# Kernel optimization log

Measured on AMD Instinct MI355X. Metric: run time of the kernel, lower is better.

## Reference

```python
import jax, jax.numpy as jnp
import numpy as np

STEPS = 200
H = 0.5
N_POP = 100000.0
CLAMP = 100000.0
BATCH = 65536


def setup_inputs() -> dict:
    key = jax.random.key(0)
    k1, k2 = jax.random.split(key)
    # init state [B, 1, 4] = (S, E, I, R); positive values
    init = jax.random.uniform(k1, (BATCH, 1, 4), dtype=jnp.float32) * 1000.0
    # weights mirrors nn.Parameter([100000, 3, 6, 0, 0.5, 0.2, 0.25]) with small noise
    base = jnp.array([100000.0, 3.0, 6.0, 0.0, 0.5, 0.2, 0.25], dtype=jnp.float32)
    weights = base + 0.01 * jax.random.normal(k2, (7,), dtype=jnp.float32)
    return {"init": init, "weights": weights}


def reference(init, weights):
    A, B, C = weights[4], weights[5], weights[6]

    def step(x, _):
        # x: [B, 1, 4]
        s, e, i = x[:, 0, 0], x[:, 0, 1], x[:, 0, 2]
        infl = B * s * (e + i) / N_POP
        d = jnp.stack((-infl, infl - A * e, A * e - C * i, C * i), axis=-1)  # [B, 4]
        x_new = x + H * jnp.clip(d[:, None, :], -CLAMP, CLAMP)  # [B, 1, 4]
        return x_new, x_new

    _, outs = jax.lax.scan(step, init, None, length=STEPS)  # [steps, B, 1, 4]
    return jnp.moveaxis(outs, 0, 1)  # [B, steps, 1, 4]
```

## Files before the change

### kernel.cpp

```cpp
#include <hip/hip_runtime.h>

#define BATCH   65536
#define STEPS   200
#define TCHUNK  8
#define NCHUNK  (STEPS / TCHUNK)
#define BLK     64
#define LSTRIDE 33

__global__ __launch_bounds__(BLK) void seir_kernel(
    const float* __restrict__ init,
    const float* __restrict__ w,
    float* __restrict__ out)
{
    __shared__ float lds[BLK * LSTRIDE];

    const int lane   = threadIdx.x;
    const int base_b = blockIdx.x * BLK;
    const int b      = base_b + lane;

    const float A = w[4];
    const float B = w[5];
    const float C = w[6];
    const float invN = 1.0f / 100000.0f;

    float4 x = reinterpret_cast<const float4*>(init)[b];
    float4* outf4 = reinterpret_cast<float4*>(out);

    for (int chunk = 0; chunk < NCHUNK; ++chunk) {
        #pragma unroll
        for (int tt = 0; tt < TCHUNK; ++tt) {
            float infl = B * x.x * (x.y + x.z) * invN;
            float ae = A * x.y;
            float ci = C * x.z;
            float d0 = -infl;
            float d1 = infl - ae;
            float d2 = ae - ci;
            float d3 = ci;
            d0 = fminf(fmaxf(d0, -100000.0f), 100000.0f);
            d1 = fminf(fmaxf(d1, -100000.0f), 100000.0f);
            d2 = fminf(fmaxf(d2, -100000.0f), 100000.0f);
            d3 = fminf(fmaxf(d3, -100000.0f), 100000.0f);
            x.x += 0.5f * d0;
            x.y += 0.5f * d1;
            x.z += 0.5f * d2;
            x.w += 0.5f * d3;
            const int a = lane * LSTRIDE + tt * 4;
            lds[a + 0] = x.x;
            lds[a + 1] = x.y;
            lds[a + 2] = x.z;
            lds[a + 3] = x.w;
        }
        __syncthreads();

        const int t0 = chunk * TCHUNK;
        #pragma unroll
        for (int k = 0; k < 8; ++k) {
            const int s  = k * BLK + lane;
            const int bb = s >> 3;
            const int j  = s & 7;
            const int a  = bb * LSTRIDE + j * 4;
            float4 v = make_float4(lds[a + 0], lds[a + 1], lds[a + 2], lds[a + 3]);
            outf4[(size_t)(base_b + bb) * STEPS + t0 + j] = v;
        }
        __syncthreads();
    }
}

extern "C" void kernel_launch(void* const* d_in, const int* in_sizes, int n_in,
                              void* d_out, int out_size, void* d_ws, size_t ws_size,
                              hipStream_t stream) {
    const float* init = (const float*)d_in[0];
    const float* w    = (const float*)d_in[1];
    float* out        = (float*)d_out;

    seir_kernel<<<dim3(BATCH / BLK), dim3(BLK), 0, stream>>>(init, w, out);
}
```

Baseline: 204.7 us.

## Split recurrence into checkpoint pass and parallel segment-replay pass

A first kernel runs the full recurrence per batch element and stores the state every 8 steps to workspace. A second kernel launches one block per (segment, batch tile), replays 8 steps from its checkpoint, and writes the output through LDS transposition. This exposes far more parallelism for the 210 MB output write than 1024 64-thread blocks looping serially. It costs an extra ~25 MB checkpoint round trip and a second launch, and falls back to the old single kernel if the workspace is too small. The multiply by 1/N is also folded into B.

New measurement: 213.6 us. 1.04x slower.

```diff
diff --git a/kernel.cpp b/kernel.cpp
--- a/kernel.cpp
+++ b/kernel.cpp
@@ -2,65 +2,117 @@
 
 #define BATCH   65536
 #define STEPS   200
-#define TCHUNK  8
-#define NCHUNK  (STEPS / TCHUNK)
-#define BLK     64
+#define SEG     8
+#define NSEG    (STEPS / SEG)
+#define NCKPT   (NSEG - 1)
 #define LSTRIDE 33
 
-__global__ __launch_bounds__(BLK) void seir_kernel(
+__device__ __forceinline__ float4 seir_step(float4 x, float A, float Binv, float C) {
+    float infl = Binv * x.x * (x.y + x.z);
+    float ae = A * x.y;
+    float ci = C * x.z;
+    float d0 = -infl;
+    float d1 = infl - ae;
+    float d2 = ae - ci;
+    float d3 = ci;
+    d0 = fminf(fmaxf(d0, -100000.0f), 100000.0f);
+    d1 = fminf(fmaxf(d1, -100000.0f), 100000.0f);
+    d2 = fminf(fmaxf(d2, -100000.0f), 100000.0f);
+    d3 = fminf(fmaxf(d3, -100000.0f), 100000.0f);
+    x.x += 0.5f * d0;
+    x.y += 0.5f * d1;
+    x.z += 0.5f * d2;
+    x.w += 0.5f * d3;
+    return x;
+}
+
+__global__ __launch_bounds__(256) void seir_phase1(
     const float* __restrict__ init,
     const float* __restrict__ w,
-    float* __restrict__ out)
+    float4* __restrict__ cp)
 {
-    __shared__ float lds[BLK * LSTRIDE];
-
-    const int lane   = threadIdx.x;
-    const int base_b = blockIdx.x * BLK;
-    const int b      = base_b + lane;
-
-    const float A = w[4];
-    const float B = w[5];
-    const float C = w[6];
-    const float invN = 1.0f / 100000.0f;
+    const int b = blockIdx.x * 256 + threadIdx.x;
+    const float A = w[4], Binv = w[5] * (1.0f / 100000.0f), C = w[6];
 
     float4 x = reinterpret_cast<const float4*>(init)[b];
-    float4* outf4 = reinterpret_cast<float4*>(out);
+    for (int k = 0; k < NCKPT; ++k) {
+        #pragma unroll
+        for (int t = 0; t < SEG; ++t) x = seir_step(x, A, Binv, C);
+        cp[(size_t)k * BATCH + b] = x;
+    }
+}
 
-    for (int chunk = 0; chunk < NCHUNK; ++chunk) {
+__global__ __launch_bounds__(256) void seir_phase2(
+    const float* __restrict__ init,
+    const float* __restrict__ w,
+    const float4* __restrict__ cp,
+    float4* __restrict__ out4)
+{
+    __shared__ float lds[256 * LSTRIDE];
+
+    const int tid  = threadIdx.x;
+    const int lane = tid & 63;
+    const int wv   = tid >> 6;
+    const int seg  = blockIdx.x >> 8;
+    const int bblk = (blockIdx.x & 255) * 256;
+    const int b    = bblk + tid;
+
+    const float A = w[4], Binv = w[5] * (1.0f / 100000.0f), C = w[6];
+
+    float4 x = (seg == 0) ? reinterpret_cast<const float4*>(init)[b]
+                          : cp[(size_t)(seg - 1) * BATCH + b];
+
+    float* wlds = lds + wv * 64 * LSTRIDE;
+
+    #pragma unroll
+    for (int t = 0; t < SEG; ++t) {
+        x = seir_step(x, A, Binv, C);
+        const int a = lane * LSTRIDE + t * 4;
+        wlds[a + 0] = x.x;
+        wlds[a + 1] = x.y;
+        wlds[a + 2] = x.z;
+        wlds[a + 3] = x.w;
+    }
+    __syncthreads();
+
+    const int wb = bblk + wv * 64;
+    const int t0 = seg * SEG;
+    #pragma unroll
+    for (int k = 0; k < 8; ++k) {
+        const int s  = k * 64 + lane;
+        const int bb = s >> 3;
+        const int j  = s & 7;
+        const int a  = bb * LSTRIDE + j * 4;
+        float4 v = make_float4(wlds[a + 0], wlds[a + 1], wlds[a + 2], wlds[a + 3]);
+        out4[(size_t)(wb + bb) * STEPS + t0 + j] = v;
+    }
+}
+
+__global__ __launch_bounds__(64) void seir_mono(
+    const float* __restrict__ init,
+    const float* __restrict__ w,
+    float4* __restrict__ out4)
+{
+    __shared__ float lds[64 * LSTRIDE];
+    const int lane   = threadIdx.x;
+    const int base_b = blockIdx.x * 64;
+    const float A = w[4], Binv = w[5] * (1.0f / 100000.0f), C = w[6];
+    float4 x = reinterpret_cast<const float4*>(init)[base_b + lane];
+    for (int chunk = 0; chunk < NSEG; ++chunk) {
         #pragma unroll
-        for (int tt = 0; tt < TCHUNK; ++tt) {
-            float infl = B * x.x * (x.y + x.z) * invN;
-            float ae = A * x.y;
-            float ci = C * x.z;
-            float d0 = -infl;
-            float d1 = infl - ae;
-            float d2 = ae - ci;
-            float d3 = ci;
-            d0 = fminf(fmaxf(d0, -100000.0f), 100000.0f);
-            d1 = fminf(fmaxf(d1, -100000.0f), 100000.0f);
-            d2 = fminf(fmaxf(d2, -100000.0f), 100000.0f);
-            d3 = fminf(fmaxf(d3, -100000.0f), 100000.0f);
-            x.x += 0.5f * d0;
-            x.y += 0.5f * d1;
-            x.z += 0.5f * d2;
-            x.w += 0.5f * d3;
+        for (int tt = 0; tt < SEG; ++tt) {
+            x = seir_step(x, A, Binv, C);
             const int a = lane * LSTRIDE + tt * 4;
-            lds[a + 0] = x.x;
-            lds[a + 1] = x.y;
-            lds[a + 2] = x.z;
-            lds[a + 3] = x.w;
+            lds[a] = x.x; lds[a + 1] = x.y; lds[a + 2] = x.z; lds[a + 3] = x.w;
         }
         __syncthreads();
-
-        const int t0 = chunk * TCHUNK;
+        const int t0 = chunk * SEG;
         #pragma unroll
         for (int k = 0; k < 8; ++k) {
-            const int s  = k * BLK + lane;
-            const int bb = s >> 3;
-            const int j  = s & 7;
-            const int a  = bb * LSTRIDE + j * 4;
-            float4 v = make_float4(lds[a + 0], lds[a + 1], lds[a + 2], lds[a + 3]);
-            outf4[(size_t)(base_b + bb) * STEPS + t0 + j] = v;
+            const int s = k * 64 + lane;
+            const int bb = s >> 3, j = s & 7, a = bb * LSTRIDE + j * 4;
+            float4 v = make_float4(lds[a], lds[a + 1], lds[a + 2], lds[a + 3]);
+            out4[(size_t)(base_b + bb) * STEPS + t0 + j] = v;
         }
         __syncthreads();
     }
@@ -71,7 +123,14 @@
                               hipStream_t stream) {
     const float* init = (const float*)d_in[0];
     const float* w    = (const float*)d_in[1];
-    float* out        = (float*)d_out;
+    float4* out4      = (float4*)d_out;
 
-    seir_kernel<<<dim3(BATCH / BLK), dim3(BLK), 0, stream>>>(init, w, out);
+    const size_t cp_bytes = (size_t)NCKPT * BATCH * sizeof(float4);
+    if (ws_size >= cp_bytes) {
+        float4* cp = (float4*)d_ws;
+        seir_phase1<<<dim3(BATCH / 256), dim3(256), 0, stream>>>(init, w, cp);
+        seir_phase2<<<dim3((BATCH / 256) * NSEG), dim3(256), 0, stream>>>(init, w, cp, out4);
+    } else {
+        seir_mono<<<dim3(BATCH / 64), dim3(64), 0, stream>>>(init, w, out4);
+    }
 }
```
